# Performance work log

Measured on AMD Instinct MI355X. Metric: run time of the kernel, lower is better.

The kernel has to match this reference:

```python
import jax, jax.numpy as jnp
import numpy as np

# ---- static config (matches init_kwargs) ----
C = 256          # in_channels
NH = 8           # num_heads
DH = 32          # dim_head
INNER = NH * DH  # 256
WD, WH, WW = 4, 8, 8   # window_size
NW = WD * WH * WW      # tokens per window = 256
SCALE = DH ** -0.5
EPS = 1e-5


def _make_rel_index():
    # Swin-3D relative position index, shape (NW, NW), values in [0, (2Wd-1)(2Wh-1)(2Ww-1))
    coords = np.stack(np.meshgrid(np.arange(WD), np.arange(WH), np.arange(WW), indexing='ij'))
    cf = coords.reshape(3, -1)                      # (3, NW)
    rel = cf[:, :, None] - cf[:, None, :]           # (3, NW, NW)
    rel = rel.transpose(1, 2, 0).astype(np.int64)   # (NW, NW, 3)
    rel[..., 0] += WD - 1
    rel[..., 1] += WH - 1
    rel[..., 2] += WW - 1
    rel[..., 0] *= (2 * WH - 1) * (2 * WW - 1)
    rel[..., 1] *= (2 * WW - 1)
    return rel.sum(-1)                              # (NW, NW)


def setup_inputs() -> dict:
    key = jax.random.key(0)
    k = jax.random.split(key, 5)
    num_rel = (2 * WD - 1) * (2 * WH - 1) * (2 * WW - 1)  # 1575
    x = jax.random.normal(k[0], (1, C, 16, 64, 64), dtype=jnp.float32)
    return {
        'x': x,
        'ln_gamma': jnp.ones((C,), jnp.float32),
        'ln_beta': jnp.zeros((C,), jnp.float32),
        'w_qkv': jax.random.normal(k[1], (C, 3 * INNER), jnp.float32) * 0.02,
        'w_out': jax.random.normal(k[2], (INNER, C), jnp.float32) * 0.02,
        'b_out': jnp.zeros((C,), jnp.float32),
        'bias_table': jax.random.normal(k[3], (num_rel, NH), jnp.float32) * 0.02,
        'rel_index': jnp.asarray(_make_rel_index(), dtype=jnp.int32),
    }


def reference(x, ln_gamma, ln_beta, w_qkv, w_out, b_out, bias_table, rel_index):
    B, Cc, D, H, W = x.shape
    Gd, Gh, Gw = D // WD, H // WH, W // WW
    # --- window partition: (B,C,D,H,W) -> (B*Gd*Gh*Gw, NW, C) ---
    xw = x.reshape(B, Cc, Gd, WD, Gh, WH, Gw, WW)
    xw = xw.transpose(0, 2, 4, 6, 3, 5, 7, 1)           # B,Gd,Gh,Gw,Wd,Wh,Ww,C
    xw = xw.reshape(B * Gd * Gh * Gw, NW, Cc)
    # --- LayerNorm over channels ---
    mu = xw.mean(-1, keepdims=True)
    var = xw.var(-1, keepdims=True)
    xn = (xw - mu) * jax.lax.rsqrt(var + EPS) * ln_gamma + ln_beta
    # --- QKV projection (no bias) ---
    qkv = xn @ w_qkv                                     # (Bp, NW, 3*INNER)
    q, k_, v = jnp.split(qkv, 3, axis=-1)
    Bp = q.shape[0]
    q = q.reshape(Bp, NW, NH, DH)
    k_ = k_.reshape(Bp, NW, NH, DH)
    v = v.reshape(Bp, NW, NH, DH)
    # --- attention with relative position bias ---
    scores = jnp.einsum('bnhd,bmhd->bhnm', q, k_) * SCALE
    bias = bias_table[rel_index]                         # (NW, NW, NH)
    scores = scores + bias.transpose(2, 0, 1)[None]      # broadcast over windows
    attn = jax.nn.softmax(scores, axis=-1)
    out = jnp.einsum('bhnm,bmhd->bnhd', attn, v).reshape(Bp, NW, INNER)
    # --- output projection (dropout p=0 is identity) ---
    out = out @ w_out + b_out
    # --- merge windows back ---
    out = out.reshape(B, Gd, Gh, Gw, WD, WH, WW, Cc)
    out = out.transpose(0, 7, 1, 4, 2, 5, 3, 6).reshape(B, Cc, D, H, W)
    return out
```

## Files before the change

### kernel.cpp

```cpp
#include <hip/hip_runtime.h>
#include <hip/hip_bf16.h>

typedef __attribute__((ext_vector_type(8))) short short8;
typedef __attribute__((ext_vector_type(4))) short s16x4;
typedef __attribute__((ext_vector_type(4))) float f32x4;
typedef __attribute__((ext_vector_type(2))) unsigned int u32x2;

#define NWIN 256
#define NW   256
#define CH   256
#define NH   8
#define DH   32
#define ATTN_SCALE 0.17677669529663687f
#define LOG2E 1.4426950408889634f
#define QSCALE (ATTN_SCALE * LOG2E)

__device__ __forceinline__ unsigned short f2bf(float f) {
  union { float f; unsigned u; } v; v.f = f;
  unsigned r = v.u + 0x7FFFu + ((v.u >> 16) & 1u);
  return (unsigned short)(r >> 16);
}
__device__ __forceinline__ float bf2f(unsigned short h) {
  union { unsigned u; float f; } v; v.u = ((unsigned)h) << 16;
  return v.f;
}
__device__ __forceinline__ int swz128(int row, int kb) { return row * 128 + (kb ^ ((row & 7) << 4)); }
__device__ __forceinline__ void gload16(const unsigned short* g, unsigned short* l) {
  __builtin_amdgcn_global_load_lds((const __attribute__((address_space(1))) unsigned int*)(g),
                                   (__attribute__((address_space(3))) unsigned int*)(l), 16, 0, 0);
}

__global__ __launch_bounds__(256) void k_prep(const float* __restrict__ wqkv,
                                              const float* __restrict__ wout,
                                              const float* __restrict__ table,
                                              const int* __restrict__ relidx,
                                              unsigned short* __restrict__ wqh,
                                              unsigned short* __restrict__ woh,
                                              unsigned short* __restrict__ wol,
                                              float* __restrict__ bias2) {
  int idx = blockIdx.x * 256 + threadIdx.x;
  int h = idx >> 16;
  int qk = idx & 65535;
  bias2[idx] = table[relidx[qk] * 8 + h] * LOG2E;
  if (idx < 196608) {
    int k = idx / 768, n = idx % 768;
    float v = wqkv[idx];
    if (n < 256) v *= QSCALE;
    wqh[n * 256 + k] = f2bf(v);
  }
  if (idx < 65536) {
    int k = idx >> 8, n = idx & 255;
    float v = wout[idx];
    unsigned short hi = f2bf(v);
    woh[n * 256 + k] = hi;
    wol[n * 256 + k] = f2bf(v - bf2f(hi));
  }
}

__global__ __launch_bounds__(256) void k_ln(const float* __restrict__ x,
                                            const float* __restrict__ gamma,
                                            const float* __restrict__ beta,
                                            unsigned short* __restrict__ xn) {
  __shared__ unsigned short buf[256][66];
  __shared__ float stats[2][16][64];
  int bid = blockIdx.x;
  int d = bid >> 6, h = bid & 63;
  int t = threadIdx.x;
  int wq = (t & 15) << 2;
  int cp = t >> 4;
  const float* xrow = x + (size_t)d * 4096 + (size_t)h * 64;
  float s0[4] = {0.f, 0.f, 0.f, 0.f}, s1[4] = {0.f, 0.f, 0.f, 0.f};
  for (int ci = 0; ci < 16; ++ci) {
    int c = ci * 16 + cp;
    f32x4 v = *(const f32x4*)(xrow + (size_t)c * 65536 + wq);
    unsigned pk01 = (unsigned)f2bf(v[0]) | ((unsigned)f2bf(v[1]) << 16);
    unsigned pk23 = (unsigned)f2bf(v[2]) | ((unsigned)f2bf(v[3]) << 16);
    *(unsigned*)&buf[c][wq]     = pk01;
    *(unsigned*)&buf[c][wq + 2] = pk23;
#pragma unroll
    for (int j = 0; j < 4; ++j) { s0[j] += v[j]; s1[j] += v[j] * v[j]; }
  }
#pragma unroll
  for (int j = 0; j < 4; ++j) { stats[0][cp][wq + j] = s0[j]; stats[1][cp][wq + j] = s1[j]; }
  __syncthreads();
  int lane = t & 63, wv = t >> 6;
  int winb = (d >> 2) * 64 + (h >> 3) * 8;
  int tokb = (d & 3) * 64 + (h & 7) * 8;
  for (int wi = 0; wi < 16; ++wi) {
    int w2 = wi * 4 + wv;
    float sum = 0.f, sq = 0.f;
#pragma unroll
    for (int i = 0; i < 16; ++i) { sum += stats[0][i][w2]; sq += stats[1][i][w2]; }
    float mu = sum * 0.00390625f;
    float var = sq * 0.00390625f - mu * mu;
    float rstd = rsqrtf(var + 1e-5f);
    int win = winb + (w2 >> 3);
    int tok = tokb + (w2 & 7);
    unsigned short* dst = xn + ((size_t)win * NW + tok) * CH;
    for (int cc = 0; cc < 4; ++cc) {
      int c = cc * 64 + lane;
      float v = bf2f(buf[c][w2]);
      dst[c] = f2bf((v - mu) * rstd * gamma[c] + beta[c]);
    }
  }
}

__global__ __launch_bounds__(256) void k_qkv(const unsigned short* __restrict__ xn,
                                             const unsigned short* __restrict__ bhi,
                                             unsigned short* __restrict__ qkvH) {
  __shared__ unsigned short sA[8192], sBh[8192];
  int t = threadIdx.x;
  int gid = blockIdx.x;
  int xcd = gid & 7, s = gid >> 3;
  int mbase = ((xcd << 6) + s / 6) << 7;
  int nbase = (s % 6) << 7;
  int wid = t >> 6, lane = t & 63;
  int wm = wid >> 1, wn = wid & 1;
  f32x4 acc[4][4];
#pragma unroll
  for (int i = 0; i < 4; ++i)
#pragma unroll
    for (int j = 0; j < 4; ++j) acc[i][j] = (f32x4)(0.f);
  for (int kt = 0; kt < 4; ++kt) {
#pragma unroll
    for (int i = 0; i < 4; ++i) {
      int ch = t + (i << 8);
      int row = ch >> 3, sl = ch & 7;
      int gs = sl ^ (row & 7);
      size_t go = (size_t)(mbase + row) * 256 + (kt << 6) + (gs << 3);
      size_t gb = (size_t)(nbase + row) * 256 + (kt << 6) + (gs << 3);
      gload16(xn + go,  sA  + ch * 8);
      gload16(bhi + gb, sBh + ch * 8);
    }
    __syncthreads();
#pragma unroll
    for (int kk = 0; kk < 2; ++kk) {
      int kb = (kk << 6) + ((lane >> 4) << 4);
      short8 a[4], bh[4];
#pragma unroll
      for (int mi = 0; mi < 4; ++mi) {
        int row = (wm << 6) + (mi << 4) + (lane & 15);
        a[mi] = *(const short8*)((char*)sA + swz128(row, kb));
      }
#pragma unroll
      for (int ni = 0; ni < 4; ++ni) {
        int row = (wn << 6) + (ni << 4) + (lane & 15);
        bh[ni] = *(const short8*)((char*)sBh + swz128(row, kb));
      }
#pragma unroll
      for (int mi = 0; mi < 4; ++mi)
#pragma unroll
        for (int ni = 0; ni < 4; ++ni)
          acc[mi][ni] = __builtin_amdgcn_mfma_f32_16x16x32_bf16(a[mi], bh[ni], acc[mi][ni], 0, 0, 0);
    }
    __syncthreads();
  }
#pragma unroll
  for (int mi = 0; mi < 4; ++mi)
#pragma unroll
    for (int ni = 0; ni < 4; ++ni)
#pragma unroll
      for (int r = 0; r < 4; ++r) {
        int m = mbase + (wm << 6) + (mi << 4) + ((lane >> 4) << 2) + r;
        int n = nbase + (wn << 6) + (ni << 4) + (lane & 15);
        int mat = n >> 8, hd = (n >> 5) & 7, dh = n & 31;
        qkvH[((size_t)(mat * 8 + hd) * 65536 + m) * 32 + dh] = f2bf(acc[mi][ni][r]);
      }
}

__global__ __launch_bounds__(256) void k_attn(const unsigned short* __restrict__ qkvH,
                                              const float* __restrict__ bias2,
                                              unsigned short* __restrict__ attnout) {
  __shared__ unsigned short Vt[8192];
  __shared__ unsigned short Kt[8192];
  int win = blockIdx.x, head = blockIdx.y;
  int t = threadIdx.x, wid = t >> 6, lane = t & 63;
  int l15 = lane & 15, g = lane >> 4;
  const unsigned short* Qg = qkvH + ((size_t)(head)      * 65536 + win * 256) * 32;
  const unsigned short* Kg = qkvH + ((size_t)(8 + head)  * 65536 + win * 256) * 32;
  const unsigned short* Vg = qkvH + ((size_t)(16 + head) * 65536 + win * 256) * 32;

  {
    const unsigned short* vrow = Vg + (size_t)t * 32;
    short8 v0 = *(const short8*)(vrow);
    short8 v1 = *(const short8*)(vrow + 8);
    short8 v2 = *(const short8*)(vrow + 16);
    short8 v3 = *(const short8*)(vrow + 24);
    int tb = t * 2;
#pragma unroll
    for (int j = 0; j < 8; ++j) {
      int sj = tb ^ (j << 4);
      *(unsigned short*)((char*)Vt + (j)      * 512 + sj)       = (unsigned short)v0[j];
      *(unsigned short*)((char*)Vt + (8 + j)  * 512 + (sj ^ 8)) = (unsigned short)v1[j];
      *(unsigned short*)((char*)Vt + (16 + j) * 512 + sj)       = (unsigned short)v2[j];
      *(unsigned short*)((char*)Vt + (24 + j) * 512 + (sj ^ 8)) = (unsigned short)v3[j];
    }
  }
  {
    const unsigned short* krow = Kg + (size_t)t * 32;
    short8 k0 = *(const short8*)(krow);
    short8 k1 = *(const short8*)(krow + 8);
    short8 k2 = *(const short8*)(krow + 16);
    short8 k3 = *(const short8*)(krow + 24);
    char* kd = (char*)Kt + t * 64;
    int ks = ((t >> 1) & 3) << 4;
    *(short8*)(kd + (0  ^ ks)) = k0;
    *(short8*)(kd + (16 ^ ks)) = k1;
    *(short8*)(kd + (32 ^ ks)) = k2;
    *(short8*)(kd + (48 ^ ks)) = k3;
  }
  short8 bq[4];
#pragma unroll
  for (int qt = 0; qt < 4; ++qt)
    bq[qt] = *(const short8*)(Qg + (size_t)(wid * 64 + qt * 16 + l15) * 32 + g * 8);

  f32x4 o[4][2];
#pragma unroll
  for (int qt = 0; qt < 4; ++qt) { o[qt][0] = (f32x4)(0.f); o[qt][1] = (f32x4)(0.f); }
  float l_[4] = {0.f, 0.f, 0.f, 0.f};
  const float* bthread = bias2 + ((size_t)head << 16) + (size_t)(wid * 64 + l15) * 256 + g * 4;
  int vswz = ((l15 & 7) << 4) ^ (l15 & 8);
  int kswz = ((l15 >> 1) & 3) << 4;

  f32x4 nb0, nb1, nb2, nb3;
  {
    const float* bp = bthread;
    nb0 = *(const f32x4*)(bp);
    nb1 = *(const f32x4*)(bp + 16);
    nb2 = *(const f32x4*)(bp + 32);
    nb3 = *(const f32x4*)(bp + 48);
  }

  __syncthreads();

  for (int ck = 0; ck < 4; ++ck) {
    short8 ak[4];
#pragma unroll
    for (int tt = 0; tt < 4; ++tt)
      ak[tt] = *(const short8*)((char*)Kt + (ck * 64 + tt * 16 + l15) * 64 + ((g * 16) ^ kswz));
#pragma unroll
    for (int qt = 0; qt < 4; ++qt) {
      f32x4 cb[4];
      cb[0] = nb0; cb[1] = nb1; cb[2] = nb2; cb[3] = nb3;
      if (!(ck == 3 && qt == 3)) {
        int nqt = (qt + 1) & 3;
        int nck = (qt == 3) ? ck + 1 : ck;
        const float* bp = bthread + (size_t)nqt * 4096 + nck * 64;
        nb0 = *(const f32x4*)(bp);
        nb1 = *(const f32x4*)(bp + 16);
        nb2 = *(const f32x4*)(bp + 32);
        nb3 = *(const f32x4*)(bp + 48);
      }
      f32x4 z[4];
      __builtin_amdgcn_s_setprio(1);
#pragma unroll
      for (int tt = 0; tt < 4; ++tt)
        z[tt] = __builtin_amdgcn_mfma_f32_16x16x32_bf16(ak[tt], bq[qt], cb[tt], 0, 0, 0);
      __builtin_amdgcn_s_setprio(0);
      u32x2 wPq[4];
#pragma unroll
      for (int tt = 0; tt < 4; ++tt) {
        float p0 = __builtin_amdgcn_exp2f(z[tt][0]);
        float p1 = __builtin_amdgcn_exp2f(z[tt][1]);
        float p2 = __builtin_amdgcn_exp2f(z[tt][2]);
        float p3 = __builtin_amdgcn_exp2f(z[tt][3]);
        l_[qt] += (p0 + p1) + (p2 + p3);
        __hip_bfloat162 lo = __float22bfloat162_rn(float2{p0, p1});
        __hip_bfloat162 hi = __float22bfloat162_rn(float2{p2, p3});
        u32x2 pk;
        pk.x = *(unsigned int*)&lo;
        pk.y = *(unsigned int*)&hi;
        wPq[tt] = pk;
      }
      __builtin_amdgcn_s_setprio(1);
#pragma unroll
      for (int tt = 0; tt < 4; ++tt) {
        int tokb = (ck * 128 + tt * 32 + g * 8) ^ vswz;
        s16x4 pa = __builtin_bit_cast(s16x4, wPq[tt]);
#pragma unroll
        for (int dht = 0; dht < 2; ++dht) {
          s16x4 vb = *(const s16x4*)((char*)Vt + (dht * 16 + l15) * 512 + tokb);
          o[qt][dht] = __builtin_amdgcn_mfma_f32_16x16x16bf16_1k(pa, vb, o[qt][dht], 0, 0, 0);
        }
      }
      __builtin_amdgcn_s_setprio(0);
    }
  }
#pragma unroll
  for (int qt = 0; qt < 4; ++qt) {
    float lq = l_[qt];
    lq += __shfl_xor(lq, 16);
    lq += __shfl_xor(lq, 32);
    float linv = 1.0f / lq;
#pragma unroll
    for (int r = 0; r < 4; ++r) {
      float lr = __shfl(linv, g * 4 + r);
      int q = wid * 64 + qt * 16 + g * 4 + r;
      unsigned short* dst = attnout + ((size_t)(win * NW + q)) * CH + head * DH + l15;
      dst[0]  = f2bf(o[qt][0][r] * lr);
      dst[16] = f2bf(o[qt][1][r] * lr);
    }
  }
}

union SmemOP {
  struct { unsigned short A[8192], Bh[8192], Bl[8192]; } st;
  float ot[64][129];
};
__global__ __launch_bounds__(256) void k_outproj(const unsigned short* __restrict__ attnout,
                                                 const unsigned short* __restrict__ bhi,
                                                 const unsigned short* __restrict__ blo,
                                                 const float* __restrict__ bo,
                                                 float* __restrict__ out) {
  __shared__ SmemOP sm;
  int t = threadIdx.x;
  int gid = blockIdx.x;
  int xcd = gid & 7, s = gid >> 3;
  int mbase = ((xcd << 6) + (s >> 1)) << 7;
  int nbase = (s & 1) << 7;
  int wid = t >> 6, lane = t & 63;
  int wm = wid >> 1, wn = wid & 1;
  f32x4 acc[4][4];
#pragma unroll
  for (int i = 0; i < 4; ++i)
#pragma unroll
    for (int j = 0; j < 4; ++j) acc[i][j] = (f32x4)(0.f);
  for (int kt = 0; kt < 4; ++kt) {
#pragma unroll
    for (int i = 0; i < 4; ++i) {
      int ch = t + (i << 8);
      int row = ch >> 3, c16 = ch & 7;
      size_t go = (size_t)(mbase + row) * 256 + (kt << 6) + (c16 << 3);
      short8 va = *(const short8*)(attnout + go);
      *(short8*)((char*)sm.st.A + swz128(row, c16 << 4)) = va;
      size_t gb = (size_t)(nbase + row) * 256 + (kt << 6) + (c16 << 3);
      short8 vh = *(const short8*)(bhi + gb);
      *(short8*)((char*)sm.st.Bh + swz128(row, c16 << 4)) = vh;
      short8 vl = *(const short8*)(blo + gb);
      *(short8*)((char*)sm.st.Bl + swz128(row, c16 << 4)) = vl;
    }
    __syncthreads();
#pragma unroll
    for (int kk = 0; kk < 2; ++kk) {
      int kb = (kk << 6) + ((lane >> 4) << 4);
      short8 a[4], bh[4], bl[4];
#pragma unroll
      for (int mi = 0; mi < 4; ++mi) {
        int row = (wm << 6) + (mi << 4) + (lane & 15);
        a[mi] = *(const short8*)((char*)sm.st.A + swz128(row, kb));
      }
#pragma unroll
      for (int ni = 0; ni < 4; ++ni) {
        int row = (wn << 6) + (ni << 4) + (lane & 15);
        bh[ni] = *(const short8*)((char*)sm.st.Bh + swz128(row, kb));
        bl[ni] = *(const short8*)((char*)sm.st.Bl + swz128(row, kb));
      }
#pragma unroll
      for (int mi = 0; mi < 4; ++mi)
#pragma unroll
        for (int ni = 0; ni < 4; ++ni) {
          acc[mi][ni] = __builtin_amdgcn_mfma_f32_16x16x32_bf16(a[mi], bh[ni], acc[mi][ni], 0, 0, 0);
          acc[mi][ni] = __builtin_amdgcn_mfma_f32_16x16x32_bf16(a[mi], bl[ni], acc[mi][ni], 0, 0, 0);
        }
    }
    __syncthreads();
  }
  int win = mbase >> 8;
  int tokbase = mbase & 255;
  int gd = win >> 6, gh = (win >> 3) & 7, gw = win & 7;
  size_t posw = (size_t)gd * 4 * 4096 + (size_t)gh * 8 * 64 + (size_t)gw * 8;
  for (int half = 0; half < 2; ++half) {
    if (wm == half) {
#pragma unroll
      for (int mi = 0; mi < 4; ++mi)
#pragma unroll
        for (int ni = 0; ni < 4; ++ni)
#pragma unroll
          for (int r = 0; r < 4; ++r)
            sm.ot[(mi << 4) + ((lane >> 4) << 2) + r][(wn << 6) + (ni << 4) + (lane & 15)] = acc[mi][ni][r];
    }
    __syncthreads();
    int tok = tokbase + half * 64 + lane;
    int td = tok >> 6, th = (tok >> 3) & 7, tw = tok & 7;
    size_t pos = posw + (size_t)td * 4096 + (size_t)th * 64 + tw;
    for (int cc = 0; cc < 32; ++cc) {
      int c = (cc << 2) + wid;
      float v = sm.ot[lane][c] + bo[nbase + c];
      out[(size_t)(nbase + c) * 65536 + pos] = v;
    }
    __syncthreads();
  }
}

extern "C" void kernel_launch(void* const* d_in, const int* in_sizes, int n_in,
                              void* d_out, int out_size, void* d_ws, size_t ws_size,
                              hipStream_t stream) {
  const float* x     = (const float*)d_in[0];
  const float* gamma = (const float*)d_in[1];
  const float* beta  = (const float*)d_in[2];
  const float* wqkv  = (const float*)d_in[3];
  const float* wout  = (const float*)d_in[4];
  const float* bout  = (const float*)d_in[5];
  const float* btab  = (const float*)d_in[6];
  const int*   ridx  = (const int*)d_in[7];
  float* out = (float*)d_out;
  char* ws = (char*)d_ws;
  unsigned short* xn   = (unsigned short*)(ws);
  unsigned short* qkv  = (unsigned short*)(ws + 33554432);
  unsigned short* wqh  = (unsigned short*)(ws + 134217728);
  unsigned short* woh  = (unsigned short*)(ws + 135004160);
  unsigned short* wol  = (unsigned short*)(ws + 135135232);
  float* bias2         = (float*)(ws + 135266304);
  unsigned short* attnout = xn;

  k_prep<<<dim3(2048), dim3(256), 0, stream>>>(wqkv, wout, btab, ridx, wqh, woh, wol, bias2);
  k_ln<<<dim3(1024), dim3(256), 0, stream>>>(x, gamma, beta, xn);
  k_qkv<<<dim3(3072), dim3(256), 0, stream>>>(xn, wqh, qkv);
  k_attn<<<dim3(256, 8), dim3(256), 0, stream>>>(qkv, bias2, attnout);
  k_outproj<<<dim3(1024), dim3(256), 0, stream>>>(attnout, woh, wol, bout, out);
}
```

Measured before the change: 181.6 us.

## Double-buffer K-tiles in QKV and out-projection GEMMs and merge prep into LayerNorm

Both GEMM kernels now use double-buffered 32-wide K tiles, loaded asynchronously into LDS with a new XOR swizzle, so the next tile's loads overlap MFMA work on the current one and each step needs one barrier instead of two. The out-projection also switches from register-staged loads to direct global-to-LDS loads. The weight and bias preparation kernel is folded into the LayerNorm launch as extra blocks, saving one kernel launch. In exchange there are more loop iterations with less MFMA work per barrier, and the new swizzle may change the LDS bank-conflict pattern.

```diff
diff --git a/kernel.cpp b/kernel.cpp
--- a/kernel.cpp
+++ b/kernel.cpp
@@ -24,48 +24,61 @@
   union { unsigned u; float f; } v; v.u = ((unsigned)h) << 16;
   return v.f;
 }
-__device__ __forceinline__ int swz128(int row, int kb) { return row * 128 + (kb ^ ((row & 7) << 4)); }
 __device__ __forceinline__ void gload16(const unsigned short* g, unsigned short* l) {
   __builtin_amdgcn_global_load_lds((const __attribute__((address_space(1))) unsigned int*)(g),
                                    (__attribute__((address_space(3))) unsigned int*)(l), 16, 0, 0);
 }
-
-__global__ __launch_bounds__(256) void k_prep(const float* __restrict__ wqkv,
-                                              const float* __restrict__ wout,
-                                              const float* __restrict__ table,
-                                              const int* __restrict__ relidx,
-                                              unsigned short* __restrict__ wqh,
-                                              unsigned short* __restrict__ woh,
-                                              unsigned short* __restrict__ wol,
-                                              float* __restrict__ bias2) {
-  int idx = blockIdx.x * 256 + threadIdx.x;
-  int h = idx >> 16;
-  int qk = idx & 65535;
-  bias2[idx] = table[relidx[qk] * 8 + h] * LOG2E;
-  if (idx < 196608) {
-    int k = idx / 768, n = idx % 768;
-    float v = wqkv[idx];
-    if (n < 256) v *= QSCALE;
-    wqh[n * 256 + k] = f2bf(v);
-  }
-  if (idx < 65536) {
-    int k = idx >> 8, n = idx & 255;
-    float v = wout[idx];
-    unsigned short hi = f2bf(v);
-    woh[n * 256 + k] = hi;
-    wol[n * 256 + k] = f2bf(v - bf2f(hi));
-  }
-}
-
-__global__ __launch_bounds__(256) void k_ln(const float* __restrict__ x,
-                                            const float* __restrict__ gamma,
-                                            const float* __restrict__ beta,
-                                            unsigned short* __restrict__ xn) {
+__device__ __forceinline__ int swz64s(int row, int g) {
+  return g ^ ((row >> 1) & 3) ^ ((row >> 3) & 3);
+}
+__device__ __forceinline__ void stage32(const unsigned short* __restrict__ gsrc,
+                                        unsigned short* __restrict__ ldst, int t) {
+#pragma unroll
+  for (int i = 0; i < 2; ++i) {
+    int ch = t + (i << 8);
+    int row = ch >> 2, s = ch & 3;
+    int gs = swz64s(row, s);
+    gload16(gsrc + (size_t)row * 256 + gs * 8, ldst + ch * 8);
+  }
+}
+
+__global__ __launch_bounds__(256) void k_lnprep(const float* __restrict__ x,
+                                                const float* __restrict__ gamma,
+                                                const float* __restrict__ beta,
+                                                const float* __restrict__ wqkv,
+                                                const float* __restrict__ wout,
+                                                const float* __restrict__ table,
+                                                const int* __restrict__ relidx,
+                                                unsigned short* __restrict__ xn,
+                                                unsigned short* __restrict__ wqh,
+                                                unsigned short* __restrict__ woh,
+                                                unsigned short* __restrict__ wol,
+                                                float* __restrict__ bias2) {
   __shared__ unsigned short buf[256][66];
   __shared__ float stats[2][16][64];
   int bid = blockIdx.x;
+  int t = threadIdx.x;
+  if (bid >= 1024) {
+    int idx = (bid - 1024) * 256 + t;
+    int h = idx >> 16;
+    int qk = idx & 65535;
+    bias2[idx] = table[relidx[qk] * 8 + h] * LOG2E;
+    if (idx < 196608) {
+      int k = idx / 768, n = idx % 768;
+      float v = wqkv[idx];
+      if (n < 256) v *= QSCALE;
+      wqh[n * 256 + k] = f2bf(v);
+    }
+    if (idx < 65536) {
+      int k = idx >> 8, n = idx & 255;
+      float v = wout[idx];
+      unsigned short hi = f2bf(v);
+      woh[n * 256 + k] = hi;
+      wol[n * 256 + k] = f2bf(v - bf2f(hi));
+    }
+    return;
+  }
   int d = bid >> 6, h = bid & 63;
-  int t = threadIdx.x;
   int wq = (t & 15) << 2;
   int cp = t >> 4;
   const float* xrow = x + (size_t)d * 4096 + (size_t)h * 64;
@@ -108,7 +121,7 @@
 __global__ __launch_bounds__(256) void k_qkv(const unsigned short* __restrict__ xn,
                                              const unsigned short* __restrict__ bhi,
                                              unsigned short* __restrict__ qkvH) {
-  __shared__ unsigned short sA[8192], sBh[8192];
+  __shared__ unsigned short sA[2][4096], sB[2][4096];
   int t = threadIdx.x;
   int gid = blockIdx.x;
   int xcd = gid & 7, s = gid >> 3;
@@ -116,43 +129,41 @@
   int nbase = (s % 6) << 7;
   int wid = t >> 6, lane = t & 63;
   int wm = wid >> 1, wn = wid & 1;
+  int l15 = lane & 15, g = lane >> 4;
   f32x4 acc[4][4];
 #pragma unroll
   for (int i = 0; i < 4; ++i)
 #pragma unroll
     for (int j = 0; j < 4; ++j) acc[i][j] = (f32x4)(0.f);
-  for (int kt = 0; kt < 4; ++kt) {
-#pragma unroll
-    for (int i = 0; i < 4; ++i) {
-      int ch = t + (i << 8);
-      int row = ch >> 3, sl = ch & 7;
-      int gs = sl ^ (row & 7);
-      size_t go = (size_t)(mbase + row) * 256 + (kt << 6) + (gs << 3);
-      size_t gb = (size_t)(nbase + row) * 256 + (kt << 6) + (gs << 3);
-      gload16(xn + go,  sA  + ch * 8);
-      gload16(bhi + gb, sBh + ch * 8);
-    }
-    __syncthreads();
-#pragma unroll
-    for (int kk = 0; kk < 2; ++kk) {
-      int kb = (kk << 6) + ((lane >> 4) << 4);
-      short8 a[4], bh[4];
-#pragma unroll
-      for (int mi = 0; mi < 4; ++mi) {
-        int row = (wm << 6) + (mi << 4) + (lane & 15);
-        a[mi] = *(const short8*)((char*)sA + swz128(row, kb));
-      }
-#pragma unroll
-      for (int ni = 0; ni < 4; ++ni) {
-        int row = (wn << 6) + (ni << 4) + (lane & 15);
-        bh[ni] = *(const short8*)((char*)sBh + swz128(row, kb));
-      }
-#pragma unroll
-      for (int mi = 0; mi < 4; ++mi)
-#pragma unroll
-        for (int ni = 0; ni < 4; ++ni)
-          acc[mi][ni] = __builtin_amdgcn_mfma_f32_16x16x32_bf16(a[mi], bh[ni], acc[mi][ni], 0, 0, 0);
-    }
+
+  const unsigned short* Abase = xn  + (size_t)mbase * 256;
+  const unsigned short* Bbase = bhi + (size_t)nbase * 256;
+  stage32(Abase, sA[0], t);
+  stage32(Bbase, sB[0], t);
+  __syncthreads();
+#pragma unroll
+  for (int kt = 0; kt < 8; ++kt) {
+    int cur = kt & 1;
+    if (kt < 7) {
+      stage32(Abase + (kt + 1) * 32, sA[cur ^ 1], t);
+      stage32(Bbase + (kt + 1) * 32, sB[cur ^ 1], t);
+    }
+    short8 a[4], bh[4];
+#pragma unroll
+    for (int mi = 0; mi < 4; ++mi) {
+      int row = (wm << 6) + (mi << 4) + l15;
+      a[mi] = *(const short8*)((char*)sA[cur] + row * 64 + (swz64s(row, g) << 4));
+    }
+#pragma unroll
+    for (int ni = 0; ni < 4; ++ni) {
+      int row = (wn << 6) + (ni << 4) + l15;
+      bh[ni] = *(const short8*)((char*)sB[cur] + row * 64 + (swz64s(row, g) << 4));
+    }
+#pragma unroll
+    for (int mi = 0; mi < 4; ++mi)
+#pragma unroll
+      for (int ni = 0; ni < 4; ++ni)
+        acc[mi][ni] = __builtin_amdgcn_mfma_f32_16x16x32_bf16(a[mi], bh[ni], acc[mi][ni], 0, 0, 0);
     __syncthreads();
   }
 #pragma unroll
@@ -304,7 +315,7 @@
 }
 
 union SmemOP {
-  struct { unsigned short A[8192], Bh[8192], Bl[8192]; } st;
+  struct { unsigned short A[2][4096], Bh[2][4096], Bl[2][4096]; } st;
   float ot[64][129];
 };
 __global__ __launch_bounds__(256) void k_outproj(const unsigned short* __restrict__ attnout,
@@ -320,49 +331,48 @@
   int nbase = (s & 1) << 7;
   int wid = t >> 6, lane = t & 63;
   int wm = wid >> 1, wn = wid & 1;
+  int l15 = lane & 15, g = lane >> 4;
   f32x4 acc[4][4];
 #pragma unroll
   for (int i = 0; i < 4; ++i)
 #pragma unroll
     for (int j = 0; j < 4; ++j) acc[i][j] = (f32x4)(0.f);
-  for (int kt = 0; kt < 4; ++kt) {
-#pragma unroll
-    for (int i = 0; i < 4; ++i) {
-      int ch = t + (i << 8);
-      int row = ch >> 3, c16 = ch & 7;
-      size_t go = (size_t)(mbase + row) * 256 + (kt << 6) + (c16 << 3);
-      short8 va = *(const short8*)(attnout + go);
-      *(short8*)((char*)sm.st.A + swz128(row, c16 << 4)) = va;
-      size_t gb = (size_t)(nbase + row) * 256 + (kt << 6) + (c16 << 3);
-      short8 vh = *(const short8*)(bhi + gb);
-      *(short8*)((char*)sm.st.Bh + swz128(row, c16 << 4)) = vh;
-      short8 vl = *(const short8*)(blo + gb);
-      *(short8*)((char*)sm.st.Bl + swz128(row, c16 << 4)) = vl;
-    }
-    __syncthreads();
-#pragma unroll
-    for (int kk = 0; kk < 2; ++kk) {
-      int kb = (kk << 6) + ((lane >> 4) << 4);
-      short8 a[4], bh[4], bl[4];
-#pragma unroll
-      for (int mi = 0; mi < 4; ++mi) {
-        int row = (wm << 6) + (mi << 4) + (lane & 15);
-        a[mi] = *(const short8*)((char*)sm.st.A + swz128(row, kb));
+
+  const unsigned short* Abase  = attnout + (size_t)mbase * 256;
+  const unsigned short* Bhbase = bhi + (size_t)nbase * 256;
+  const unsigned short* Blbase = blo + (size_t)nbase * 256;
+  stage32(Abase,  sm.st.A[0],  t);
+  stage32(Bhbase, sm.st.Bh[0], t);
+  stage32(Blbase, sm.st.Bl[0], t);
+  __syncthreads();
+#pragma unroll
+  for (int kt = 0; kt < 8; ++kt) {
+    int cur = kt & 1;
+    if (kt < 7) {
+      stage32(Abase  + (kt + 1) * 32, sm.st.A[cur ^ 1],  t);
+      stage32(Bhbase + (kt + 1) * 32, sm.st.Bh[cur ^ 1], t);
+      stage32(Blbase + (kt + 1) * 32, sm.st.Bl[cur ^ 1], t);
+    }
+    short8 a[4], bh[4], bl[4];
+#pragma unroll
+    for (int mi = 0; mi < 4; ++mi) {
+      int row = (wm << 6) + (mi << 4) + l15;
+      a[mi] = *(const short8*)((char*)sm.st.A[cur] + row * 64 + (swz64s(row, g) << 4));
+    }
+#pragma unroll
+    for (int ni = 0; ni < 4; ++ni) {
+      int row = (wn << 6) + (ni << 4) + l15;
+      int off = row * 64 + (swz64s(row, g) << 4);
+      bh[ni] = *(const short8*)((char*)sm.st.Bh[cur] + off);
+      bl[ni] = *(const short8*)((char*)sm.st.Bl[cur] + off);
+    }
+#pragma unroll
+    for (int mi = 0; mi < 4; ++mi)
+#pragma unroll
+      for (int ni = 0; ni < 4; ++ni) {
+        acc[mi][ni] = __builtin_amdgcn_mfma_f32_16x16x32_bf16(a[mi], bh[ni], acc[mi][ni], 0, 0, 0);
+        acc[mi][ni] = __builtin_amdgcn_mfma_f32_16x16x32_bf16(a[mi], bl[ni], acc[mi][ni], 0, 0, 0);
       }
-#pragma unroll
-      for (int ni = 0; ni < 4; ++ni) {
-        int row = (wn << 6) + (ni << 4) + (lane & 15);
-        bh[ni] = *(const short8*)((char*)sm.st.Bh + swz128(row, kb));
-        bl[ni] = *(const short8*)((char*)sm.st.Bl + swz128(row, kb));
-      }
-#pragma unroll
-      for (int mi = 0; mi < 4; ++mi)
-#pragma unroll
-        for (int ni = 0; ni < 4; ++ni) {
-          acc[mi][ni] = __builtin_amdgcn_mfma_f32_16x16x32_bf16(a[mi], bh[ni], acc[mi][ni], 0, 0, 0);
-          acc[mi][ni] = __builtin_amdgcn_mfma_f32_16x16x32_bf16(a[mi], bl[ni], acc[mi][ni], 0, 0, 0);
-        }
-    }
     __syncthreads();
   }
   int win = mbase >> 8;
@@ -413,8 +423,8 @@
   float* bias2         = (float*)(ws + 135266304);
   unsigned short* attnout = xn;
 
-  k_prep<<<dim3(2048), dim3(256), 0, stream>>>(wqkv, wout, btab, ridx, wqh, woh, wol, bias2);
-  k_ln<<<dim3(1024), dim3(256), 0, stream>>>(x, gamma, beta, xn);
+  k_lnprep<<<dim3(3072), dim3(256), 0, stream>>>(x, gamma, beta, wqkv, wout, btab, ridx,
+                                                 xn, wqh, woh, wol, bias2);
   k_qkv<<<dim3(3072), dim3(256), 0, stream>>>(xn, wqh, qkv);
   k_attn<<<dim3(256, 8), dim3(256), 0, stream>>>(qkv, bias2, attnout);
   k_outproj<<<dim3(1024), dim3(256), 0, stream>>>(attnout, woh, wol, bout, out);
```

Result: no change. 184.1 us, median of 2 (+1.4%).
